# Optimization experiments

Hardware: AMD Instinct MI355X
Metric: run time of the kernel (lower is better)

The kernel has to match this reference:

```python
import jax, jax.numpy as jnp
import numpy as np

D_MODEL = 1024
NUM_HEADS = 16
D_KEY = D_MODEL // NUM_HEADS


def setup_inputs() -> dict:
    key = jax.random.key(0)
    ks = jax.random.split(key, 9)
    B, S = 2, 2048
    s = 1.0 / np.sqrt(D_MODEL)
    return {
        "x": jax.random.normal(ks[0], (B, S, D_MODEL), dtype=jnp.float32),
        "W_q": jax.random.normal(ks[1], (D_MODEL, D_MODEL), dtype=jnp.float32) * s,
        "b_q": jnp.zeros((D_MODEL,), dtype=jnp.float32),
        "W_k": jax.random.normal(ks[2], (D_MODEL, D_MODEL), dtype=jnp.float32) * s,
        "b_k": jnp.zeros((D_MODEL,), dtype=jnp.float32),
        "W_v": jax.random.normal(ks[3], (D_MODEL, D_MODEL), dtype=jnp.float32) * s,
        "b_v": jnp.zeros((D_MODEL,), dtype=jnp.float32),
        "W_o": jax.random.normal(ks[4], (D_MODEL, D_MODEL), dtype=jnp.float32) * s,
        "b_o": jnp.zeros((D_MODEL,), dtype=jnp.float32),
    }


def reference(x, W_q, b_q, W_k, b_k, W_v, b_v, W_o, b_o):
    B, S, _ = x.shape
    # Linear projections (torch nn.Linear: x @ W.T + b; here W stored as [in, out])
    Q = x @ W_q + b_q
    K = x @ W_k + b_k
    V = x @ W_v + b_v
    # [B, S, H, dk] -> [B, H, S, dk]
    def split_heads(t):
        return t.reshape(B, S, NUM_HEADS, D_KEY).transpose(0, 2, 1, 3)
    Q, K, V = split_heads(Q), split_heads(K), split_heads(V)
    scale = 1.0 / np.sqrt(D_KEY).astype(np.float32)
    logits = jnp.einsum("bhqd,bhkd->bhqk", Q, K) * scale  # [B,H,S,S]
    weights = jax.nn.softmax(logits, axis=-1)
    ctx = jnp.einsum("bhqk,bhkd->bhqd", weights, V)       # [B,H,S,dk]
    concat = ctx.transpose(0, 2, 1, 3).reshape(B, S, D_MODEL)
    return concat @ W_o + b_o
```

## Files before the change

kernel.cpp:

```cpp
#include <hip/hip_runtime.h>
#include <cstdint>
#include <cstddef>

#define SEQ   2048
#define NH    16
#define DK    64
#define DM    1024
#define MTOT  4096
#define QSCALE (0.125f * 1.44269504088896f)

typedef __attribute__((ext_vector_type(8))) short           short8;
typedef __attribute__((ext_vector_type(8))) unsigned short  ushort8;
typedef __attribute__((ext_vector_type(4))) unsigned short  ushort4v;
typedef __attribute__((ext_vector_type(2))) unsigned int    uint2v;
typedef __attribute__((ext_vector_type(4))) unsigned int    uint4v;
typedef __attribute__((ext_vector_type(4))) float           float4v;
typedef unsigned short u16;
typedef unsigned int   u32;

__device__ inline float4v mfma16(short8 a, short8 b, float4v c) {
    return __builtin_amdgcn_mfma_f32_16x16x32_bf16(a, b, c, 0, 0, 0);
}
__device__ inline u16 f2bf(float f) {
    u32 u = __float_as_uint(f);
    u += 0x7fffu + ((u >> 16) & 1u);
    return (u16)(u >> 16);
}
__device__ inline u32 pkbf(float a, float b) {
    u32 r;
    asm("v_cvt_pk_bf16_f32 %0, %1, %2" : "=v"(r) : "v"(a), "v"(b));
    return r;
}
__device__ inline float ex2(float x) {
    float r;
    asm("v_exp_f32 %0, %1" : "=v"(r) : "v"(x));
    return r;
}
__device__ inline void pl32swap(u32& a, u32& b) {
    asm("v_permlane32_swap_b32 %0, %1" : "+v"(a), "+v"(b));
}
__device__ inline void pl16swap(u32& a, u32& b) {
    asm("v_permlane16_swap_b32 %0, %1" : "+v"(a), "+v"(b));
}
__device__ inline void gld16(const void* g, void* lds) {
    __builtin_amdgcn_global_load_lds(
        (const __attribute__((address_space(1))) u32*)g,
        (__attribute__((address_space(3))) u32*)lds, 16, 0, 0);
}

__global__ __launch_bounds__(256)
void prep(const float* __restrict__ x, u16* __restrict__ xb,
          const float* __restrict__ W0, const float* __restrict__ W1,
          const float* __restrict__ W2, const float* __restrict__ W3,
          u16* __restrict__ T0, u16* __restrict__ T1,
          u16* __restrict__ T2, u16* __restrict__ T3)
{
    __shared__ u16 t[64][68];
    if (blockIdx.x < 2048) {
        const int i = blockIdx.x * 256 + threadIdx.x;
        const float4v a = ((const float4v*)x)[2 * i];
        const float4v b = ((const float4v*)x)[2 * i + 1];
        ushort8 o;
        #pragma unroll
        for (int j = 0; j < 4; j++) { o[j] = f2bf(a[j]); o[4 + j] = f2bf(b[j]); }
        ((ushort8*)xb)[i] = o;
        return;
    }
    const int bi = blockIdx.x - 2048;
    const int bx = bi & 15, by = (bi >> 4) & 15, bz = bi >> 8;
    const float* W; u16* T;
    switch (bz) {
        case 0: W = W0; T = T0; break;
        case 1: W = W1; T = T1; break;
        case 2: W = W2; T = T2; break;
        default: W = W3; T = T3; break;
    }
    const int n0 = bx * 64, k0 = by * 64;
    const int r  = threadIdx.x >> 4;
    const int c4 = (threadIdx.x & 15) * 4;
    #pragma unroll
    for (int i = 0; i < 4; i++) {
        float4v v = *(const float4v*)&W[(size_t)(k0 + r + i * 16) * DM + n0 + c4];
        #pragma unroll
        for (int j = 0; j < 4; j++) t[r + i * 16][c4 + j] = f2bf(v[j]);
    }
    __syncthreads();
    #pragma unroll
    for (int i = 0; i < 4; i++) {
        const int rr = r + i * 16;
        ushort4v o;
        #pragma unroll
        for (int j = 0; j < 4; j++) o[j] = t[c4 + j][rr];
        *(ushort4v*)&T[(size_t)(n0 + rr) * DM + k0 + c4] = o;
    }
}

template<int TM, int BN, int MODE>
__global__ __launch_bounds__(512)
void gemm_bt(const u16* __restrict__ A, const u16* __restrict__ WT,
             const float* __restrict__ bq, const float* __restrict__ bk,
             const float* __restrict__ bv,
             void* __restrict__ out0, u16* __restrict__ outK, u16* __restrict__ outV)
{
    constexpr int NT = 512;
    constexpr int MF = TM / 32;
    constexpr int NF = BN / 64;
    __shared__ u16 Al[2][TM][64];
    __shared__ u16 Bl[2][BN][64];
    const int tid  = threadIdx.x;
    const int lane = tid & 63, w = tid >> 6;
    const int quad = lane >> 4, l16 = lane & 15;

    const int nxb  = gridDim.x;
    const int wgid = blockIdx.y * nxb + blockIdx.x;
    const int per  = (nxb * gridDim.y) >> 3;
    const int nl   = (wgid & 7) * per + (wgid >> 3);
    const int n0 = (nl % nxb) * BN, m0 = (nl / nxb) * TM;

    const int wm = (w >> 2) * (TM / 2);
    const int wn = (w & 3) * (BN / 4);

    float4v acc[MF][NF] = {};

    auto STAGE = [&](int k0, int buf) {
        #pragma unroll
        for (int j = 0; j < TM * 8 / NT; j++) {
            const int c = j * NT + tid;
            const int row = c >> 3, kc = c & 7;
            gld16(A + (size_t)(m0 + row) * DM + k0 + ((kc ^ (row & 7)) * 8),
                  &Al[buf][0][0] + (size_t)(j * NT + w * 64) * 8);
        }
        #pragma unroll
        for (int j = 0; j < BN * 8 / NT; j++) {
            const int c = j * NT + tid;
            const int row = c >> 3, kc = c & 7;
            gld16(WT + (size_t)(n0 + row) * DM + k0 + ((kc ^ (row & 7)) * 8),
                  &Bl[buf][0][0] + (size_t)(j * NT + w * 64) * 8);
        }
    };

    STAGE(0, 0);
    for (int ks = 0; ks < DM / 64; ++ks) {
        const int buf = ks & 1;
        __syncthreads();
        if (ks + 1 < DM / 64) STAGE((ks + 1) * 64, buf ^ 1);
        #pragma unroll
        for (int u = 0; u < 2; u++) {
            short8 af[MF], bf[NF];
            #pragma unroll
            for (int mi = 0; mi < MF; mi++) {
                const int row = wm + mi * 16 + l16;
                af[mi] = *(const short8*)&Al[buf][row][((4 * u + quad) ^ (row & 7)) * 8];
            }
            #pragma unroll
            for (int ni = 0; ni < NF; ni++) {
                const int row = wn + ni * 16 + l16;
                bf[ni] = *(const short8*)&Bl[buf][row][((4 * u + quad) ^ (row & 7)) * 8];
            }
            __builtin_amdgcn_s_setprio(1);
            #pragma unroll
            for (int mi = 0; mi < MF; mi++)
                #pragma unroll
                for (int ni = 0; ni < NF; ni++)
                    acc[mi][ni] = mfma16(af[mi], bf[ni], acc[mi][ni]);
            __builtin_amdgcn_s_setprio(0);
        }
    }

    if constexpr (MODE == 0) {
        float* out = (float*)out0;
        #pragma unroll
        for (int ni = 0; ni < NF; ni++) {
            const int col = n0 + wn + ni * 16 + l16;
            const float bb = bq[col];
            #pragma unroll
            for (int mi = 0; mi < MF; mi++)
                #pragma unroll
                for (int r = 0; r < 4; r++) {
                    const int row = m0 + wm + mi * 16 + quad * 4 + r;
                    out[(size_t)row * DM + col] = acc[mi][ni][r] + bb;
                }
        }
    } else {
        #pragma unroll
        for (int ni = 0; ni < NF; ni++) {
            const int colg = n0 + wn + ni * 16 + l16;
            const int seg  = colg >> 10;
            u16* outp = (seg == 0) ? (u16*)out0 : (seg == 1 ? outK : outV);
            const float* bias = (seg == 0) ? bq : (seg == 1 ? bk : bv);
            const int col = colg & 1023;
            const float bb = bias[col];
            const int h = col >> 6, d = col & 63;
            if (seg < 2) {
                const float scl = (seg == 0) ? QSCALE : 1.0f;
                #pragma unroll
                for (int mi = 0; mi < MF; mi++)
                    #pragma unroll
                    for (int r = 0; r < 4; r++) {
                        const int row = m0 + wm + mi * 16 + quad * 4 + r;
                        const int b = row >> 11, s = row & (SEQ - 1);
                        outp[(((size_t)(b * NH + h) * SEQ + s) << 6) + d] =
                            f2bf((acc[mi][ni][r] + bb) * scl);
                    }
            } else {
                #pragma unroll
                for (int mi = 0; mi < MF; mi++) {
                    const int row0 = m0 + wm + mi * 16 + quad * 4;
                    const int b = row0 >> 11, s = row0 & (SEQ - 1);
                    uint2v pv;
                    pv[0] = pkbf(acc[mi][ni][0] + bb, acc[mi][ni][1] + bb);
                    pv[1] = pkbf(acc[mi][ni][2] + bb, acc[mi][ni][3] + bb);
                    *(uint2v*)&outp[(((size_t)((b * NH + h) * DK + d)) << 11) + s] = pv;
                }
            }
        }
    }
}

__global__ __launch_bounds__(512, 4)
void attn_kernel(const u16* __restrict__ Q, const u16* __restrict__ K,
                 const u16* __restrict__ VT, u16* __restrict__ Ctx)
{
    __shared__ __align__(16) u16 pool[32768];

    const int tid  = threadIdx.x;
    const int lane = tid & 63, w = tid >> 6;
    const int wq = w & 3, wgrp = w >> 2;
    const int quad = lane >> 4, l16 = lane & 15;

    const int wgid = blockIdx.y * 16 + blockIdx.x;
    const int nlin = (wgid & 7) * 64 + (wgid >> 3);
    const int qt = nlin & 15;
    const int bh = nlin >> 4;
    const size_t head = (size_t)bh * SEQ * DK;

    short8 qf[2][2];
    #pragma unroll
    for (int g = 0; g < 2; g++) {
        const size_t qrow = head + (size_t)(qt * 128 + wq * 32 + g * 16 + l16) * DK;
        qf[g][0] = *(const short8*)(Q + qrow + quad * 8);
        qf[g][1] = *(const short8*)(Q + qrow + 32 + quad * 8);
    }

    float4v acc[2][4] = {};
    float l_part[2] = {0.f, 0.f};

    const int sh = tid >> 8;
    const int rK = (tid >> 3) & 31, cK = tid & 7;
    const int dV = (tid >> 2) & 63, cV = tid & 3;
    const int sVk = (dV & 3) ^ ((dV >> 2) & 3);
    const u16* const Kg = K  + head + (size_t)(sh * 1024 + rK) * DK + (cK ^ (rK & 7)) * 8;
    const u16* const Vg = VT + head + (size_t)dV * SEQ + sh * 1024 + (cV ^ sVk) * 8;
    u16* const Kdst = pool + tid * 8;
    u16* const Vdst = pool + 16384 + tid * 8;

    auto QKSTEP = [&](int cur, float4v znew[2][2]) {
        short8 kf[2][2];
        #pragma unroll
        for (int t = 0; t < 2; t++) {
            const int row = t * 16 + l16;
            const u16* kb = pool + cur * 4096 + wgrp * 2048 + row * 64;
            kf[t][0] = *(const short8*)(kb + (quad ^ (row & 7)) * 8);
            kf[t][1] = *(const short8*)(kb + ((4 + quad) ^ (row & 7)) * 8);
        }
        __builtin_amdgcn_s_setprio(1);
        #pragma unroll
        for (int t = 0; t < 2; t++)
            #pragma unroll
            for (int g = 0; g < 2; g++) {
                float4v zz = {};
                zz = mfma16(kf[t][0], qf[g][0], zz);
                zz = mfma16(kf[t][1], qf[g][1], zz);
                znew[t][g] = zz;
            }
        __builtin_amdgcn_s_setprio(0);
    };

    auto SMPACK = [&](float4v zp[2][2], short8 pf[2]) {
        #pragma unroll
        for (int g = 0; g < 2; g++) {
            float p[2][4];
            #pragma unroll
            for (int t = 0; t < 2; t++) {
                p[t][0] = ex2(zp[t][g][0]); p[t][1] = ex2(zp[t][g][1]);
                p[t][2] = ex2(zp[t][g][2]); p[t][3] = ex2(zp[t][g][3]);
                l_part[g] += (p[t][0] + p[t][1]) + (p[t][2] + p[t][3]);
            }
            u32 A = pkbf(p[0][0], p[0][1]);
            u32 B = pkbf(p[0][2], p[0][3]);
            u32 C = pkbf(p[1][0], p[1][1]);
            u32 D = pkbf(p[1][2], p[1][3]);
            pl32swap(A, C); pl16swap(A, C);
            pl32swap(B, D); pl16swap(B, D);
            uint4v pw; pw[0] = A; pw[1] = B; pw[2] = C; pw[3] = D;
            pf[g] = __builtin_bit_cast(short8, pw);
        }
    };

    auto PVSTEP = [&](int pv, short8 pf[2]) {
        __builtin_amdgcn_s_setprio(1);
        #pragma unroll
        for (int t = 0; t < 4; t++) {
            const int d = t * 16 + l16;
            const u16* vb = pool + 16384 + pv * 4096 + wgrp * 2048 + d * 32;
            const short8 vf =
                *(const short8*)(vb + (quad ^ ((d & 3) ^ ((d >> 2) & 3))) * 8);
            acc[0][t] = mfma16(vf, pf[0], acc[0][t]);
            acc[1][t] = mfma16(vf, pf[1], acc[1][t]);
        }
        __builtin_amdgcn_s_setprio(0);
    };

    gld16(Kg,                 Kdst);
    gld16(Vg,                 Vdst);
    gld16(Kg + 32 * DK,       Kdst + 4096);
    gld16(Vg + 32,            Vdst + 4096);

    float4v zp[2][2];

    __syncthreads();
    gld16(Kg + (size_t)2 * 32 * DK, Kdst + 2 * 4096);
    gld16(Vg + (size_t)2 * 32,      Vdst + 2 * 4096);
    QKSTEP(0, zp);

    for (int it = 1; it < 32; ++it) {
        const int cur = it & 3, pv = (it - 1) & 3;
        __syncthreads();
        if (it + 2 < 32) {
            gld16(Kg + (size_t)(it + 2) * 32 * DK, Kdst + ((it + 2) & 3) * 4096);
            gld16(Vg + (size_t)(it + 2) * 32,      Vdst + ((it + 2) & 3) * 4096);
        }
        float4v zn[2][2];
        QKSTEP(cur, zn);
        short8 pf[2];
        SMPACK(zp, pf);
        PVSTEP(pv, pf);
        #pragma unroll
        for (int t = 0; t < 2; t++)
            #pragma unroll
            for (int g = 0; g < 2; g++) zp[t][g] = zn[t][g];
    }
    {
        short8 pf[2];
        SMPACK(zp, pf);
        PVSTEP(3, pf);
    }

    #pragma unroll
    for (int g = 0; g < 2; g++) {
        l_part[g] += __shfl_xor(l_part[g], 16);
        l_part[g] += __shfl_xor(l_part[g], 32);
    }

    float* const Xlp = (float*)pool;
    #define XL(a, b, c) Xlp[(((a) * 64 + (b)) * 17) + (c)]
    float ltot[2];
    #pragma unroll
    for (int p = 0; p < 2; p++) {
        __syncthreads();
        if (wgrp == 1) {
            #pragma unroll
            for (int g = 0; g < 2; g++)
                #pragma unroll
                for (int tt = 0; tt < 2; tt++)
                    #pragma unroll
                    for (int r = 0; r < 4; r++)
                        XL(wq, lane, g * 8 + tt * 4 + r) = acc[g][2 * p + tt][r];
            XL(wq, lane, 16) = l_part[p];
        }
        __syncthreads();
        if (wgrp == 0) {
            #pragma unroll
            for (int g = 0; g < 2; g++)
                #pragma unroll
                for (int tt = 0; tt < 2; tt++)
                    #pragma unroll
                    for (int r = 0; r < 4; r++)
                        acc[g][2 * p + tt][r] += XL(wq, lane, g * 8 + tt * 4 + r);
            ltot[p] = l_part[p] + XL(wq, lane, 16);
        }
    }
    #undef XL

    if (wgrp == 0) {
        const int b = bh >> 4, h = bh & 15;
        #pragma unroll
        for (int g = 0; g < 2; g++) {
            const float rl = 1.0f / ltot[g];
            const int s = qt * 128 + wq * 32 + g * 16 + l16;
            u16* dst = Ctx + (size_t)(b * SEQ + s) * DM + h * 64 + quad * 4;
            #pragma unroll
            for (int t = 0; t < 4; t++) {
                uint2v ov;
                ov[0] = pkbf(acc[g][t][0] * rl, acc[g][t][1] * rl);
                ov[1] = pkbf(acc[g][t][2] * rl, acc[g][t][3] * rl);
                *(uint2v*)&dst[t * 16] = ov;
            }
        }
    }
}

extern "C" void kernel_launch(void* const* d_in, const int* in_sizes, int n_in,
                              void* d_out, int out_size, void* d_ws, size_t ws_size,
                              hipStream_t stream)
{
    const float* x   = (const float*)d_in[0];
    const float* W_q = (const float*)d_in[1];
    const float* b_q = (const float*)d_in[2];
    const float* W_k = (const float*)d_in[3];
    const float* b_k = (const float*)d_in[4];
    const float* W_v = (const float*)d_in[5];
    const float* b_v = (const float*)d_in[6];
    const float* W_o = (const float*)d_in[7];
    const float* b_o = (const float*)d_in[8];

    u16* xb  = (u16*)d_ws;
    u16* WT  = xb + (size_t)MTOT * DM;
    u16* WTo = WT + (size_t)3 * DM * DM;
    u16* VTb = WTo + (size_t)DM * DM;
    u16* Cb  = xb;
    u16* Qb  = (u16*)d_out;
    u16* Kb  = Qb + (size_t)MTOT * DM;

    prep<<<3072, 256, 0, stream>>>(x, xb, W_q, W_k, W_v, W_o,
                                   WT, WT + (size_t)DM * DM,
                                   WT + (size_t)2 * DM * DM, WTo);
    gemm_bt<128, 192, 1><<<dim3(16, 32), 512, 0, stream>>>(
        xb, WT, b_q, b_k, b_v, Qb, Kb, VTb);
    attn_kernel<<<dim3(SEQ / 128, 2 * NH), 512, 0, stream>>>(Qb, Kb, VTb, Cb);
    gemm_bt<64, 128, 0><<<dim3(8, 64), 512, 0, stream>>>(
        Cb, WTo, b_o, nullptr, nullptr, (float*)d_out, nullptr, nullptr);
}
```

Before: 175.2 us.

## Fuse all four stages into one persistent kernel with grid barriers

Merges the conversion/transpose, QKV GEMM, attention, and output GEMM into a single 512-block kernel whose stages are separated by atomic-counter grid barriers in workspace. This removes three kernel launch gaps and the tail idle between dependent launches. The cost is a shared 80KB LDS footprint for every stage, which may lower occupancy for attention compared with its standalone launch, plus barrier spin time. The barrier relies on all 512 blocks being co-resident, or it deadlocks. A fallback four-kernel path is kept for when the workspace is too small.

```diff
diff --git a/kernel.cpp b/kernel.cpp
--- a/kernel.cpp
+++ b/kernel.cpp
@@ -48,75 +48,91 @@
         (__attribute__((address_space(3))) u32*)lds, 16, 0, 0);
 }
 
-__global__ __launch_bounds__(256)
-void prep(const float* __restrict__ x, u16* __restrict__ xb,
-          const float* __restrict__ W0, const float* __restrict__ W1,
-          const float* __restrict__ W2, const float* __restrict__ W3,
-          u16* __restrict__ T0, u16* __restrict__ T1,
-          u16* __restrict__ T2, u16* __restrict__ T3)
-{
-    __shared__ u16 t[64][68];
-    if (blockIdx.x < 2048) {
-        const int i = blockIdx.x * 256 + threadIdx.x;
-        const float4v a = ((const float4v*)x)[2 * i];
-        const float4v b = ((const float4v*)x)[2 * i + 1];
-        ushort8 o;
-        #pragma unroll
-        for (int j = 0; j < 4; j++) { o[j] = f2bf(a[j]); o[4 + j] = f2bf(b[j]); }
-        ((ushort8*)xb)[i] = o;
-        return;
-    }
-    const int bi = blockIdx.x - 2048;
-    const int bx = bi & 15, by = (bi >> 4) & 15, bz = bi >> 8;
-    const float* W; u16* T;
-    switch (bz) {
-        case 0: W = W0; T = T0; break;
-        case 1: W = W1; T = T1; break;
-        case 2: W = W2; T = T2; break;
-        default: W = W3; T = T3; break;
-    }
-    const int n0 = bx * 64, k0 = by * 64;
-    const int r  = threadIdx.x >> 4;
-    const int c4 = (threadIdx.x & 15) * 4;
-    #pragma unroll
-    for (int i = 0; i < 4; i++) {
-        float4v v = *(const float4v*)&W[(size_t)(k0 + r + i * 16) * DM + n0 + c4];
-        #pragma unroll
-        for (int j = 0; j < 4; j++) t[r + i * 16][c4 + j] = f2bf(v[j]);
-    }
+__device__ inline void gridbar(u32* __restrict__ bar, int idx)
+{
     __syncthreads();
-    #pragma unroll
-    for (int i = 0; i < 4; i++) {
-        const int rr = r + i * 16;
-        ushort4v o;
-        #pragma unroll
-        for (int j = 0; j < 4; j++) o[j] = t[c4 + j][rr];
-        *(ushort4v*)&T[(size_t)(n0 + rr) * DM + k0 + c4] = o;
+    if (threadIdx.x == 0) {
+        __threadfence();
+        __hip_atomic_fetch_add(&bar[idx * 32], 1u, __ATOMIC_RELAXED,
+                               __HIP_MEMORY_SCOPE_AGENT);
+        while (__hip_atomic_load(&bar[idx * 32], __ATOMIC_RELAXED,
+                                 __HIP_MEMORY_SCOPE_AGENT) < 512u)
+            __builtin_amdgcn_s_sleep(2);
+        __threadfence();
+    }
+    __syncthreads();
+}
+
+__device__ __forceinline__ void prep_body(
+    u16* __restrict__ smem, const float* __restrict__ x, u16* __restrict__ xb,
+    const float* __restrict__ W0, const float* __restrict__ W1,
+    const float* __restrict__ W2, const float* __restrict__ W3,
+    u16* __restrict__ T0, u16* __restrict__ T1,
+    u16* __restrict__ T2, u16* __restrict__ T3, const int wgid)
+{
+    {
+        const int base = (wgid * 512 + (int)threadIdx.x) * 2;
+        #pragma unroll
+        for (int j = 0; j < 2; j++) {
+            const int i = base + j;
+            const float4v a = ((const float4v*)x)[2 * i];
+            const float4v b = ((const float4v*)x)[2 * i + 1];
+            ushort8 o;
+            #pragma unroll
+            for (int q = 0; q < 4; q++) { o[q] = f2bf(a[q]); o[4 + q] = f2bf(b[q]); }
+            ((ushort8*)xb)[i] = o;
+        }
+    }
+    {
+        const int ti = wgid * 2 + ((int)threadIdx.x >> 8);
+        const int bx = ti & 15, by = (ti >> 4) & 15, bz = ti >> 8;
+        const float* W = (bz == 0) ? W0 : (bz == 1) ? W1 : (bz == 2) ? W2 : W3;
+        u16* T        = (bz == 0) ? T0 : (bz == 1) ? T1 : (bz == 2) ? T2 : T3;
+        u16* const t  = smem + ((int)threadIdx.x >> 8) * (64 * 68);
+        const int tt = threadIdx.x & 255;
+        const int r  = tt >> 4;
+        const int c4 = (tt & 15) * 4;
+        #pragma unroll
+        for (int i2 = 0; i2 < 4; i2++) {
+            float4v v = *(const float4v*)&W[(size_t)(by * 64 + r + i2 * 16) * DM
+                                            + bx * 64 + c4];
+            #pragma unroll
+            for (int j = 0; j < 4; j++) t[(r + i2 * 16) * 68 + c4 + j] = f2bf(v[j]);
+        }
+        __syncthreads();
+        #pragma unroll
+        for (int i2 = 0; i2 < 4; i2++) {
+            const int rr = r + i2 * 16;
+            ushort4v o;
+            #pragma unroll
+            for (int j = 0; j < 4; j++) o[j] = t[(c4 + j) * 68 + rr];
+            *(ushort4v*)&T[(size_t)(bx * 64 + rr) * DM + by * 64 + c4] = o;
+        }
     }
 }
 
 template<int TM, int BN, int MODE>
-__global__ __launch_bounds__(512)
-void gemm_bt(const u16* __restrict__ A, const u16* __restrict__ WT,
-             const float* __restrict__ bq, const float* __restrict__ bk,
-             const float* __restrict__ bv,
-             void* __restrict__ out0, u16* __restrict__ outK, u16* __restrict__ outV)
-{
-    constexpr int NT = 512;
-    constexpr int MF = TM / 32;
-    constexpr int NF = BN / 64;
-    __shared__ u16 Al[2][TM][64];
-    __shared__ u16 Bl[2][BN][64];
+__device__ __forceinline__ void gemm_body(
+    u16* __restrict__ smem,
+    const u16* __restrict__ A, const u16* __restrict__ WTp,
+    const float* __restrict__ bq, const float* __restrict__ bk,
+    const float* __restrict__ bv,
+    void* __restrict__ out0, u16* __restrict__ outK, u16* __restrict__ outV,
+    const int wgid, const int nxb)
+{
+    constexpr int NT  = 512;
+    constexpr int MF  = TM / 32;
+    constexpr int NF  = BN / 64;
+    constexpr int ASZ = TM * 64;
+    constexpr int BSZ = BN * 64;
+    u16* const AlB = smem;
+    u16* const BlB = smem + 2 * ASZ;
     const int tid  = threadIdx.x;
     const int lane = tid & 63, w = tid >> 6;
     const int quad = lane >> 4, l16 = lane & 15;
 
-    const int nxb  = gridDim.x;
-    const int wgid = blockIdx.y * nxb + blockIdx.x;
-    const int per  = (nxb * gridDim.y) >> 3;
-    const int nl   = (wgid & 7) * per + (wgid >> 3);
+    const int nl = (wgid & 7) * 64 + (wgid >> 3);
     const int n0 = (nl % nxb) * BN, m0 = (nl / nxb) * TM;
-
     const int wm = (w >> 2) * (TM / 2);
     const int wn = (w & 3) * (BN / 4);
 
@@ -128,14 +144,14 @@
             const int c = j * NT + tid;
             const int row = c >> 3, kc = c & 7;
             gld16(A + (size_t)(m0 + row) * DM + k0 + ((kc ^ (row & 7)) * 8),
-                  &Al[buf][0][0] + (size_t)(j * NT + w * 64) * 8);
+                  AlB + buf * ASZ + (size_t)(j * NT + w * 64) * 8);
         }
         #pragma unroll
         for (int j = 0; j < BN * 8 / NT; j++) {
             const int c = j * NT + tid;
             const int row = c >> 3, kc = c & 7;
-            gld16(WT + (size_t)(n0 + row) * DM + k0 + ((kc ^ (row & 7)) * 8),
-                  &Bl[buf][0][0] + (size_t)(j * NT + w * 64) * 8);
+            gld16(WTp + (size_t)(n0 + row) * DM + k0 + ((kc ^ (row & 7)) * 8),
+                  BlB + buf * BSZ + (size_t)(j * NT + w * 64) * 8);
         }
     };
 
@@ -150,12 +166,14 @@
             #pragma unroll
             for (int mi = 0; mi < MF; mi++) {
                 const int row = wm + mi * 16 + l16;
-                af[mi] = *(const short8*)&Al[buf][row][((4 * u + quad) ^ (row & 7)) * 8];
+                af[mi] = *(const short8*)(AlB + buf * ASZ + row * 64
+                                          + ((4 * u + quad) ^ (row & 7)) * 8);
             }
             #pragma unroll
             for (int ni = 0; ni < NF; ni++) {
                 const int row = wn + ni * 16 + l16;
-                bf[ni] = *(const short8*)&Bl[buf][row][((4 * u + quad) ^ (row & 7)) * 8];
+                bf[ni] = *(const short8*)(BlB + buf * BSZ + row * 64
+                                          + ((4 * u + quad) ^ (row & 7)) * 8);
             }
             __builtin_amdgcn_s_setprio(1);
             #pragma unroll
@@ -217,18 +235,15 @@
     }
 }
 
-__global__ __launch_bounds__(512, 4)
-void attn_kernel(const u16* __restrict__ Q, const u16* __restrict__ K,
-                 const u16* __restrict__ VT, u16* __restrict__ Ctx)
-{
-    __shared__ __align__(16) u16 pool[32768];
-
+__device__ __forceinline__ void attn_body(
+    u16* __restrict__ pool, const u16* __restrict__ Q, const u16* __restrict__ K,
+    const u16* __restrict__ VT, u16* __restrict__ Ctx, const int wgid)
+{
     const int tid  = threadIdx.x;
     const int lane = tid & 63, w = tid >> 6;
     const int wq = w & 3, wgrp = w >> 2;
     const int quad = lane >> 4, l16 = lane & 15;
 
-    const int wgid = blockIdx.y * 16 + blockIdx.x;
     const int nlin = (wgid & 7) * 64 + (wgid >> 3);
     const int qt = nlin & 15;
     const int bh = nlin >> 4;
@@ -311,10 +326,10 @@
         __builtin_amdgcn_s_setprio(0);
     };
 
-    gld16(Kg,                 Kdst);
-    gld16(Vg,                 Vdst);
-    gld16(Kg + 32 * DK,       Kdst + 4096);
-    gld16(Vg + 32,            Vdst + 4096);
+    gld16(Kg,           Kdst);
+    gld16(Vg,           Vdst);
+    gld16(Kg + 32 * DK, Kdst + 4096);
+    gld16(Vg + 32,      Vdst + 4096);
 
     float4v zp[2][2];
 
@@ -398,6 +413,67 @@
             }
         }
     }
+}
+
+__global__ __launch_bounds__(512, 4)
+void fused_mha(const float* __restrict__ x,
+               const float* __restrict__ W0, const float* __restrict__ W1,
+               const float* __restrict__ W2, const float* __restrict__ W3,
+               const float* __restrict__ bq, const float* __restrict__ bk,
+               const float* __restrict__ bv, const float* __restrict__ bo,
+               u16* xb, u16* WT, u16* WTo, u16* VTb,
+               u16* Qb, u16* Kb, u16* Cb, float* out, u32* bar)
+{
+    __shared__ __align__(16) u16 smem[40960];
+    const int wgid = blockIdx.x;
+
+    prep_body(smem, x, xb, W0, W1, W2, W3,
+              WT, WT + (size_t)DM * DM, WT + (size_t)2 * DM * DM, WTo, wgid);
+    gridbar(bar, 0);
+    gemm_body<128, 192, 1>(smem, xb, WT, bq, bk, bv, Qb, Kb, VTb, wgid, 16);
+    gridbar(bar, 1);
+    attn_body(smem, Qb, Kb, VTb, Cb, wgid);
+    gridbar(bar, 2);
+    gemm_body<64, 128, 0>(smem, Cb, WTo, bo, nullptr, nullptr,
+                          out, nullptr, nullptr, wgid, 8);
+}
+
+__global__ __launch_bounds__(512)
+void prep_k(const float* __restrict__ x, u16* __restrict__ xb,
+            const float* __restrict__ W0, const float* __restrict__ W1,
+            const float* __restrict__ W2, const float* __restrict__ W3,
+            u16* T0, u16* T1, u16* T2, u16* T3)
+{
+    __shared__ __align__(16) u16 smem[8704];
+    prep_body(smem, x, xb, W0, W1, W2, W3, T0, T1, T2, T3, blockIdx.x);
+}
+
+__global__ __launch_bounds__(512)
+void qkv_k(const u16* __restrict__ A, const u16* __restrict__ WTp,
+           const float* __restrict__ bq, const float* __restrict__ bk,
+           const float* __restrict__ bv,
+           u16* outQ, u16* outK, u16* outV)
+{
+    __shared__ __align__(16) u16 smem[40960];
+    gemm_body<128, 192, 1>(smem, A, WTp, bq, bk, bv, outQ, outK, outV,
+                           blockIdx.x, 16);
+}
+
+__global__ __launch_bounds__(512, 4)
+void attn_k(const u16* __restrict__ Q, const u16* __restrict__ K,
+            const u16* __restrict__ VT, u16* __restrict__ Ctx)
+{
+    __shared__ __align__(16) u16 pool[32768];
+    attn_body(pool, Q, K, VT, Ctx, blockIdx.x);
+}
+
+__global__ __launch_bounds__(512)
+void oproj_k(const u16* __restrict__ A, const u16* __restrict__ WTp,
+             const float* __restrict__ bo, float* out)
+{
+    __shared__ __align__(16) u16 smem[24576];
+    gemm_body<64, 128, 0>(smem, A, WTp, bo, nullptr, nullptr,
+                          out, nullptr, nullptr, blockIdx.x, 8);
 }
 
 extern "C" void kernel_launch(void* const* d_in, const int* in_sizes, int n_in,
@@ -422,12 +498,19 @@
     u16* Qb  = (u16*)d_out;
     u16* Kb  = Qb + (size_t)MTOT * DM;
 
-    prep<<<3072, 256, 0, stream>>>(x, xb, W_q, W_k, W_v, W_o,
-                                   WT, WT + (size_t)DM * DM,
-                                   WT + (size_t)2 * DM * DM, WTo);
-    gemm_bt<128, 192, 1><<<dim3(16, 32), 512, 0, stream>>>(
-        xb, WT, b_q, b_k, b_v, Qb, Kb, VTb);
-    attn_kernel<<<dim3(SEQ / 128, 2 * NH), 512, 0, stream>>>(Qb, Kb, VTb, Cb);
-    gemm_bt<64, 128, 0><<<dim3(8, 64), 512, 0, stream>>>(
-        Cb, WTo, b_o, nullptr, nullptr, (float*)d_out, nullptr, nullptr);
-}
+    const size_t BASE = (size_t)24 * 1024 * 1024;
+    if (ws_size >= BASE + 512) {
+        u32* bar = (u32*)((char*)d_ws + BASE);
+        hipMemsetAsync(bar, 0, 512, stream);
+        fused_mha<<<512, 512, 0, stream>>>(
+            x, W_q, W_k, W_v, W_o, b_q, b_k, b_v, b_o,
+            xb, WT, WTo, VTb, Qb, Kb, Cb, (float*)d_out, bar);
+    } else {
+        prep_k<<<512, 512, 0, stream>>>(x, xb, W_q, W_k, W_v, W_o,
+                                        WT, WT + (size_t)DM * DM,
+                                        WT + (size_t)2 * DM * DM, WTo);
+        qkv_k<<<512, 512, 0, stream>>>(xb, WT, b_q, b_k, b_v, Qb, Kb, VTb);
+        attn_k<<<512, 512, 0, stream>>>(Qb, Kb, VTb, Cb);
+        oproj_k<<<512, 512, 0, stream>>>(Cb, WTo, b_o, (float*)d_out);
+    }
+}
```

New measurement: 351.7 us. 2.01x slower.

## Switch attention K/V staging to double-buffered 64-key tiles per barrier

Applied to the files above, without the earlier changes.

Replaces the 4-slot ring of 32-key K/V tiles, which issued one barrier per tile and carried the QK result across iterations in software, with a 2-slot double buffer of 64-key tiles. Each iteration now runs two QK sub-steps and then two softmax/PV sub-steps after a single barrier. This halves the number of barriers and removes the carried-over logits registers. The cost is a shallower prefetch distance (one tile ahead instead of two), and QK is no longer overlapped with the previous tile's softmax.

```diff
diff --git a/kernel.cpp b/kernel.cpp
--- a/kernel.cpp
+++ b/kernel.cpp
@@ -245,21 +245,30 @@
     float4v acc[2][4] = {};
     float l_part[2] = {0.f, 0.f};
 
-    const int sh = tid >> 8;
-    const int rK = (tid >> 3) & 31, cK = tid & 7;
+    const int rK = tid >> 3, cK = tid & 7;
+    const int sV = (tid >> 8) & 1;
     const int dV = (tid >> 2) & 63, cV = tid & 3;
     const int sVk = (dV & 3) ^ ((dV >> 2) & 3);
-    const u16* const Kg = K  + head + (size_t)(sh * 1024 + rK) * DK + (cK ^ (rK & 7)) * 8;
-    const u16* const Vg = VT + head + (size_t)dV * SEQ + sh * 1024 + (cV ^ sVk) * 8;
+    const u16* const Kg = K  + head + (size_t)rK * DK + (cK ^ (rK & 7)) * 8;
+    const u16* const Vg = VT + head + (size_t)dV * SEQ + sV * 32 + (cV ^ sVk) * 8;
     u16* const Kdst = pool + tid * 8;
     u16* const Vdst = pool + 16384 + tid * 8;
 
-    auto QKSTEP = [&](int cur, float4v znew[2][2]) {
+    auto STAGE = [&](int tile, int buf) {
+        const size_t ko = (size_t)tile * 64 * DK;
+        const size_t vo = (size_t)tile * 64;
+        gld16(Kg + ko,                      Kdst + buf * 8192);
+        gld16(Kg + ko + (size_t)1024 * DK,  Kdst + buf * 8192 + 4096);
+        gld16(Vg + vo,                      Vdst + buf * 8192);
+        gld16(Vg + vo + 1024,               Vdst + buf * 8192 + 4096);
+    };
+
+    auto QKSTEP = [&](int buf, int sub, float4v z[2][2]) {
         short8 kf[2][2];
         #pragma unroll
         for (int t = 0; t < 2; t++) {
             const int row = t * 16 + l16;
-            const u16* kb = pool + cur * 4096 + wgrp * 2048 + row * 64;
+            const u16* kb = pool + buf * 8192 + wgrp * 4096 + (sub * 32 + row) * 64;
             kf[t][0] = *(const short8*)(kb + (quad ^ (row & 7)) * 8);
             kf[t][1] = *(const short8*)(kb + ((4 + quad) ^ (row & 7)) * 8);
         }
@@ -271,7 +280,7 @@
                 float4v zz = {};
                 zz = mfma16(kf[t][0], qf[g][0], zz);
                 zz = mfma16(kf[t][1], qf[g][1], zz);
-                znew[t][g] = zz;
+                z[t][g] = zz;
             }
         __builtin_amdgcn_s_setprio(0);
     };
@@ -297,12 +306,13 @@
         }
     };
 
-    auto PVSTEP = [&](int pv, short8 pf[2]) {
+    auto PVSTEP = [&](int buf, int sub, short8 pf[2]) {
         __builtin_amdgcn_s_setprio(1);
         #pragma unroll
         for (int t = 0; t < 4; t++) {
             const int d = t * 16 + l16;
-            const u16* vb = pool + 16384 + pv * 4096 + wgrp * 2048 + d * 32;
+            const u16* vb = pool + 16384 + buf * 8192 + wgrp * 4096
+                          + sub * 2048 + d * 32;
             const short8 vf =
                 *(const short8*)(vb + (quad ^ ((d & 3) ^ ((d >> 2) & 3))) * 8);
             acc[0][t] = mfma16(vf, pf[0], acc[0][t]);
@@ -311,39 +321,19 @@
         __builtin_amdgcn_s_setprio(0);
     };
 
-    gld16(Kg,                 Kdst);
-    gld16(Vg,                 Vdst);
-    gld16(Kg + 32 * DK,       Kdst + 4096);
-    gld16(Vg + 32,            Vdst + 4096);
-
-    float4v zp[2][2];
-
-    __syncthreads();
-    gld16(Kg + (size_t)2 * 32 * DK, Kdst + 2 * 4096);
-    gld16(Vg + (size_t)2 * 32,      Vdst + 2 * 4096);
-    QKSTEP(0, zp);
-
-    for (int it = 1; it < 32; ++it) {
-        const int cur = it & 3, pv = (it - 1) & 3;
+    STAGE(0, 0);
+    for (int it = 0; it < 16; ++it) {
+        const int buf = it & 1;
         __syncthreads();
-        if (it + 2 < 32) {
-            gld16(Kg + (size_t)(it + 2) * 32 * DK, Kdst + ((it + 2) & 3) * 4096);
-            gld16(Vg + (size_t)(it + 2) * 32,      Vdst + ((it + 2) & 3) * 4096);
-        }
-        float4v zn[2][2];
-        QKSTEP(cur, zn);
+        if (it + 1 < 16) STAGE(it + 1, buf ^ 1);
+        float4v z0[2][2], z1[2][2];
+        QKSTEP(buf, 0, z0);
+        QKSTEP(buf, 1, z1);
         short8 pf[2];
-        SMPACK(zp, pf);
-        PVSTEP(pv, pf);
-        #pragma unroll
-        for (int t = 0; t < 2; t++)
-            #pragma unroll
-            for (int g = 0; g < 2; g++) zp[t][g] = zn[t][g];
-    }
-    {
-        short8 pf[2];
-        SMPACK(zp, pf);
-        PVSTEP(3, pf);
+        SMPACK(z0, pf);
+        PVSTEP(buf, 0, pf);
+        SMPACK(z1, pf);
+        PVSTEP(buf, 1, pf);
     }
 
     #pragma unroll
```

Result: no change. 174.7 us, median of 2 (-0.3%).
